# Kernel tuning notes

Hardware: AMD Instinct MI355X
Metric: run time of the kernel (lower is better)

## Reference

```python
import jax, jax.numpy as jnp
import numpy as np

D_IN = 1024
D_OUT = 1024


def setup_inputs() -> dict:
    key = jax.random.key(0)
    ks = jax.random.split(key, 7)
    B, S = 4, 2048
    x = jax.random.normal(ks[0], (B, S, D_IN), dtype=jnp.float32)
    s = 1.0 / np.sqrt(D_IN)
    Wq = jax.random.uniform(ks[1], (D_IN, D_OUT), jnp.float32, -s, s)
    Wk = jax.random.uniform(ks[2], (D_IN, D_OUT), jnp.float32, -s, s)
    Wv = jax.random.uniform(ks[3], (D_IN, D_OUT), jnp.float32, -s, s)
    bq = jax.random.uniform(ks[4], (D_OUT,), jnp.float32, -s, s)
    bk = jax.random.uniform(ks[5], (D_OUT,), jnp.float32, -s, s)
    bv = jax.random.uniform(ks[6], (D_OUT,), jnp.float32, -s, s)
    return {"x": x, "Wq": Wq, "Wk": Wk, "Wv": Wv, "bq": bq, "bk": bk, "bv": bv}


def reference(x, Wq, Wk, Wv, bq, bk, bv):
    # x: [B, S, d_in]
    B, S, _ = x.shape
    q = x @ Wq + bq            # [B, S, d_out]
    k = x @ Wk + bk
    v = x @ Wv + bv
    scale = 1.0 / jnp.sqrt(jnp.asarray(q.shape[-1], q.dtype))
    scores = jnp.einsum('bqd,bkd->bqk', q, k)  # [B, S, S]
    causal = jnp.tril(jnp.ones((S, S), dtype=bool))
    scores = jnp.where(causal, scores, -jnp.inf)
    attn = jax.nn.softmax(scores * scale, axis=-1)
    return jnp.einsum('bqk,bkd->bqd', attn, v)
```

## Files before the change

kernel.cpp:

```cpp
#include <hip/hip_runtime.h>
#include <cstdint>

#define DEV __device__ __forceinline__

typedef __attribute__((ext_vector_type(4))) float f32x4;
typedef __attribute__((ext_vector_type(8))) short short8;
typedef __attribute__((ext_vector_type(4))) unsigned short u16x4;

constexpr int BS  = 4;
constexpr int SEQ = 2048;

DEV ushort f2b(float f){
  uint32_t u = __builtin_bit_cast(uint32_t, f);
  u += 0x7fffu + ((u >> 16) & 1u);
  return (ushort)(u >> 16);
}
DEV float b2f(ushort h){
  uint32_t u = (uint32_t)h << 16;
  return __builtin_bit_cast(float, u);
}

DEV void gload_lds16(const void* g, void* l){
  __builtin_amdgcn_global_load_lds(
      (const __attribute__((address_space(1))) unsigned int*)g,
      (__attribute__((address_space(3))) unsigned int*)l, 16, 0, 0);
}

#define BAR()    __builtin_amdgcn_s_barrier()
#define PRIO(x)  __builtin_amdgcn_s_setprio(x)
#define SCHEDB() __builtin_amdgcn_sched_barrier(0)
#define LGKM0()  asm volatile("s_waitcnt lgkmcnt(0)" ::: "memory")
#define WAITV4() asm volatile("s_waitcnt vmcnt(4)" ::: "memory")

__global__ __launch_bounds__(256) void convert_f2b8(const float* __restrict__ src,
                                                    ushort* __restrict__ dst){
  long i = (long)blockIdx.x * 256 + threadIdx.x;
  const f32x4* s4 = (const f32x4*)src;
  f32x4 a = s4[i*2], b = s4[i*2+1];
  short8 o;
  o[0]=(short)f2b(a[0]); o[1]=(short)f2b(a[1]); o[2]=(short)f2b(a[2]); o[3]=(short)f2b(a[3]);
  o[4]=(short)f2b(b[0]); o[5]=(short)f2b(b[1]); o[6]=(short)f2b(b[2]); o[7]=(short)f2b(b[3]);
  ((short8*)dst)[i] = o;
}

__global__ __launch_bounds__(256) void transpose_f2b(const float* __restrict__ src,
                                                     ushort* __restrict__ dst,
                                                     int R, int C){
  __shared__ float t[32][33];
  int c0 = blockIdx.x * 32, r0 = blockIdx.y * 32;
  int tx = threadIdx.x, ty = threadIdx.y;
  #pragma unroll
  for (int k=0;k<4;k++) t[ty+k*8][tx] = src[(long)(r0+ty+k*8)*C + c0+tx];
  __syncthreads();
  #pragma unroll
  for (int k=0;k<4;k++) dst[(long)(c0+ty+k*8)*R + r0+tx] = f2b(t[tx][ty+k*8]);
}

__global__ __launch_bounds__(256) void transpose_b2b(const ushort* __restrict__ src,
                                                     ushort* __restrict__ dst,
                                                     int R, int C){
  __shared__ ushort t[32][33];
  int c0 = blockIdx.x * 32, r0 = blockIdx.y * 32;
  int tx = threadIdx.x, ty = threadIdx.y;
  #pragma unroll
  for (int k=0;k<4;k++) t[ty+k*8][tx] = src[(long)(r0+ty+k*8)*C + c0+tx];
  __syncthreads();
  #pragma unroll
  for (int k=0;k<4;k++) dst[(long)(c0+ty+k*8)*R + r0+tx] = t[tx][ty+k*8];
}

struct GArgs {
  const ushort* A;  long lda; long aBS;
  const ushort* Bm; long ldb; long bBS;
  void* C;          long ldc; long cBS;
  const float* b0; const float* b1; const float* b2;
  int K;
};

__global__ __launch_bounds__(512, 2) void gemmA_qkv(GArgs g){
  extern __shared__ char sm[];
  const int tid = threadIdx.x;
  const int wid = tid >> 6, lane = tid & 63;
  const int wr = wid >> 2, wc = wid & 3;
  const int lr = lane & 15, lk = lane >> 4;
  const int f5 = ((lr >> 3) & 1) << 5;

  int fid = blockIdx.x;
  int swz = (fid & 7) * 48 + (fid >> 3);
  const int m0 = (swz & 31) * 256;
  const int n0 = (swz >> 5) * 256;

  const long lda2 = g.lda * 2, ldb2 = g.ldb * 2;
  const int sr  = tid >> 2;
  const int scb = (lane & 3) << 4;
  const int scbp = scb ^ (((sr >> 3) & 1) << 5);
  const char* ar0 = (const char*)g.A  + (long)(m0 + sr      )*lda2 + scbp;
  const char* ar1 = (const char*)g.A  + (long)(m0 + 128 + sr)*lda2 + scbp;
  const char* br0 = (const char*)g.Bm + (long)(n0 + sr      )*ldb2 + scbp;
  const char* br1 = (const char*)g.Bm + (long)(n0 + 128 + sr)*ldb2 + scbp;
  const int dwo = wid << 10;

  auto ST = [&](const char* row, int c, int off, int k0){
    const char* p = row + k0*2;
    char* d = sm + c*65536 + off + dwo;
    gload_lds16(p,      d);
    gload_lds16(p + 64, d + 8192);
  };

  const int aoffs = wr*16384 + lr*64 + ((lk*16) ^ f5);
  const int boffs = 32768 + (wc>>1)*16384 + ((wc&1)*64 + lr)*64 + ((lk*16) ^ f5);

  f32x4 acc[8][4];
  #pragma unroll
  for (int m=0;m<8;m++)
    #pragma unroll
    for (int n=0;n<4;n++) acc[m][n] = f32x4{0.f,0.f,0.f,0.f};

  const int NT = g.K >> 6;
  ST(ar0, 0, 0, 0);     ST(ar1, 0, 16384, 0);
  ST(br0, 0, 32768, 0); ST(br1, 0, 49152, 0);
  ST(br0, 1, 32768, 64); ST(br1, 1, 49152, 64);
  WAITV4(); BAR();

  for (int t = 0; t < NT; ++t){
    const int c = t & 1;
    const char* base = sm + c*65536;
    const int kA = ((t+1) < NT ? (t+1) : NT-1) << 6;
    const int kB = ((t+2) < NT ? (t+2) : NT-1) << 6;
    short8 bf[4][2], af[2][2];
    ST(ar0, c^1, 0, kA); ST(ar1, c^1, 16384, kA);
    #pragma unroll
    for (int n=0;n<4;n++)
      #pragma unroll
      for (int kk=0;kk<2;kk++)
        bf[n][kk] = *(const short8*)(base + boffs + kk*8192 + n*1024);
    #pragma unroll
    for (int mm=0;mm<2;mm++)
      #pragma unroll
      for (int kk=0;kk<2;kk++)
        af[mm][kk] = *(const short8*)(base + aoffs + kk*8192 + mm*1024);
    LGKM0(); SCHEDB();
    PRIO(1);
    #pragma unroll
    for (int kk=0;kk<2;kk++)
      #pragma unroll
      for (int mm=0;mm<2;mm++)
        #pragma unroll
        for (int n=0;n<4;n++)
          acc[mm][n] = __builtin_amdgcn_mfma_f32_16x16x32_bf16(af[mm][kk], bf[n][kk], acc[mm][n], 0,0,0);
    PRIO(0);
    BAR();
    #pragma unroll
    for (int p=1;p<4;p++){
      if (p == 1) ST(br0, c, 32768, kB);
      if (p == 2) ST(br1, c, 49152, kB);
      #pragma unroll
      for (int mm=0;mm<2;mm++)
        #pragma unroll
        for (int kk=0;kk<2;kk++)
          af[mm][kk] = *(const short8*)(base + aoffs + kk*8192 + (p*2+mm)*1024);
      LGKM0(); SCHEDB();
      PRIO(1);
      #pragma unroll
      for (int kk=0;kk<2;kk++)
        #pragma unroll
        for (int mm=0;mm<2;mm++)
          #pragma unroll
          for (int n=0;n<4;n++)
            acc[p*2+mm][n] = __builtin_amdgcn_mfma_f32_16x16x32_bf16(af[mm][kk], bf[n][kk], acc[p*2+mm][n], 0,0,0);
      PRIO(0);
      if (p == 3) WAITV4();
      BAR();
    }
  }

  int sel = n0 >> 10;
  const float* bp = (sel == 0) ? g.b0 : (sel == 1) ? g.b1 : g.b2;
  ushort* Cq = (ushort*)g.C + (long)sel * 8388608;
  #pragma unroll
  for (int m=0;m<8;m++){
    int row0 = m0 + wr*128 + m*16 + lk*4;
    #pragma unroll
    for (int n=0;n<4;n++){
      int col  = n0 + wc*64 + n*16 + lr;
      int colq = col & 1023;
      float bv = bp[colq];
      #pragma unroll
      for (int i=0;i<4;i++)
        Cq[(long)(row0+i)*1024 + colq] = f2b(acc[m][n][i] + bv);
    }
  }
}

template<int MODE>
__global__ __launch_bounds__(512, 2) void gemmB(GArgs g){
  extern __shared__ char sm[];
  const int m0 = blockIdx.x * 128, n0 = blockIdx.y * 256;
  const int z  = blockIdx.z;
  if (MODE == 1 && n0 > m0 + 127) return;
  const int tid = threadIdx.x;
  const int wid = tid >> 6, lane = tid & 63;
  const int wr = wid >> 2, wc = wid & 3;
  const int lr = lane & 15, lk = lane >> 4;
  const int f5 = ((lr >> 3) & 1) << 5;

  const char* Ab = (const char*)(g.A  + (long)z * g.aBS);
  const char* Bb = (const char*)(g.Bm + (long)z * g.bBS);
  const long lda2 = g.lda * 2, ldb2 = g.ldb * 2;
  const int sr  = tid >> 2;
  const int scb = (lane & 3) << 4;
  const int scbp = scb ^ (((sr >> 3) & 1) << 5);
  const char* ar0 = Ab + (long)(m0 + sr)*lda2 + scbp;
  const char* br0 = Bb + (long)(n0 + sr      )*ldb2 + scbp;
  const char* br1 = Bb + (long)(n0 + 128 + sr)*ldb2 + scbp;
  const int dwo = wid << 10;

  auto ST = [&](const char* row, int c, int off, int k0){
    const char* p = row + k0*2;
    char* d = sm + c*49152 + off + dwo;
    gload_lds16(p,      d);
    gload_lds16(p + 64, d + 8192);
  };

  const int aoffs = (wr*64 + lr)*64 + ((lk*16) ^ f5);
  const int boffs = 16384 + (wc>>1)*16384 + ((wc&1)*64 + lr)*64 + ((lk*16) ^ f5);

  f32x4 acc[4][4];
  #pragma unroll
  for (int m=0;m<4;m++)
    #pragma unroll
    for (int n=0;n<4;n++) acc[m][n] = f32x4{0.f,0.f,0.f,0.f};

  const int Keff = (MODE == 2) ? (m0 + 128) : g.K;
  const int NT = Keff >> 6;
  ST(ar0, 0, 0, 0);
  ST(br0, 0, 16384, 0); ST(br1, 0, 32768, 0);
  ST(br0, 1, 16384, 64); ST(br1, 1, 32768, 64);
  WAITV4(); BAR();

  for (int t = 0; t < NT; ++t){
    const int c = t & 1;
    const char* base = sm + c*49152;
    const int kA = ((t+1) < NT ? (t+1) : NT-1) << 6;
    const int kB = ((t+2) < NT ? (t+2) : NT-1) << 6;
    short8 bf[4][2], af[2][2];
    ST(ar0, c^1, 0, kA);
    #pragma unroll
    for (int n=0;n<4;n++)
      #pragma unroll
      for (int kk=0;kk<2;kk++)
        bf[n][kk] = *(const short8*)(base + boffs + kk*8192 + n*1024);
    #pragma unroll
    for (int mm=0;mm<2;mm++)
      #pragma unroll
      for (int kk=0;kk<2;kk++)
        af[mm][kk] = *(const short8*)(base + aoffs + kk*8192 + mm*1024);
    LGKM0(); SCHEDB();
    PRIO(1);
    #pragma unroll
    for (int kk=0;kk<2;kk++)
      #pragma unroll
      for (int mm=0;mm<2;mm++)
        #pragma unroll
        for (int n=0;n<4;n++)
          acc[mm][n] = __builtin_amdgcn_mfma_f32_16x16x32_bf16(af[mm][kk], bf[n][kk], acc[mm][n], 0,0,0);
    PRIO(0);
    BAR();
    ST(br0, c, 16384, kB); ST(br1, c, 32768, kB);
    #pragma unroll
    for (int mm=0;mm<2;mm++)
      #pragma unroll
      for (int kk=0;kk<2;kk++)
        af[mm][kk] = *(const short8*)(base + aoffs + kk*8192 + (2+mm)*1024);
    LGKM0(); SCHEDB();
    PRIO(1);
    #pragma unroll
    for (int kk=0;kk<2;kk++)
      #pragma unroll
      for (int mm=0;mm<2;mm++)
        #pragma unroll
        for (int n=0;n<4;n++)
          acc[2+mm][n] = __builtin_amdgcn_mfma_f32_16x16x32_bf16(af[mm][kk], bf[n][kk], acc[2+mm][n], 0,0,0);
    PRIO(0);
    WAITV4();
    BAR();
  }

  long cz = (long)z * g.cBS;
  #pragma unroll
  for (int m=0;m<4;m++){
    int row0 = m0 + wr*64 + m*16 + lk*4;
    #pragma unroll
    for (int n=0;n<4;n++){
      int col = n0 + wc*64 + n*16 + lr;
      #pragma unroll
      for (int i=0;i<4;i++){
        long off = cz + (long)(row0+i)*g.ldc + col;
        if (MODE == 1) ((ushort*)g.C)[off] = f2b(acc[m][n][i]);
        else           ((float*)g.C)[off]  = acc[m][n][i];
      }
    }
  }
}

__global__ __launch_bounds__(256) void softmax_causal_b(const ushort* __restrict__ sc,
                                                        ushort* __restrict__ P){
  int row = blockIdx.x & (SEQ-1);
  int b   = blockIdx.x >> 11;
  const short8* srow = (const short8*)(sc + ((long)b*SEQ + row)*(long)SEQ);
  ushort* prow = P + ((long)b*SEQ + row)*(long)SEQ;
  int tid = threadIdx.x;
  int lane = tid & 63, wid = tid >> 6;
  const float scale = 0.03125f;
  float x[8]; float mx = -INFINITY;
  int base = tid * 8;
  if (base <= row){
    short8 v = srow[tid];
    #pragma unroll
    for (int j=0;j<8;j++){
      float t = (base + j <= row) ? b2f((ushort)v[j]) : -INFINITY;
      x[j] = t; mx = fmaxf(mx, t);
    }
  } else {
    #pragma unroll
    for (int j=0;j<8;j++) x[j] = -INFINITY;
  }
  #pragma unroll
  for (int off=1; off<64; off<<=1) mx = fmaxf(mx, __shfl_xor(mx, off));
  __shared__ float rb[8];
  if (lane == 0) rb[wid] = mx;
  __syncthreads();
  mx = fmaxf(fmaxf(rb[0],rb[1]), fmaxf(rb[2],rb[3]));
  float sum = 0.f; float e[8];
  #pragma unroll
  for (int i=0;i<8;i++){ e[i] = __expf((x[i]-mx)*scale); sum += e[i]; }
  #pragma unroll
  for (int off=1; off<64; off<<=1) sum += __shfl_xor(sum, off);
  if (lane == 0) rb[4+wid] = sum;
  __syncthreads();
  sum = (rb[4]+rb[5]) + (rb[6]+rb[7]);
  float inv = 1.0f / sum;
  int wlim = row | 127;
  if (base <= wlim){
    short8 o;
    #pragma unroll
    for (int j=0;j<8;j++) o[j] = (short)f2b(e[j]*inv);
    ((short8*)prow)[tid] = o;
  }
}

extern "C" void kernel_launch(void* const* d_in, const int* in_sizes, int n_in,
                              void* d_out, int out_size, void* d_ws, size_t ws_size,
                              hipStream_t stream){
  const float* x  = (const float*)d_in[0];
  const float* Wq = (const float*)d_in[1];
  const float* Wk = (const float*)d_in[2];
  const float* Wv = (const float*)d_in[3];
  const float* bq = (const float*)d_in[4];
  const float* bk = (const float*)d_in[5];
  const float* bv = (const float*)d_in[6];
  float* out = (float*)d_out;

  const long XB = 0;
  const long WT = 16777216;
  const long QB = 23068672;
  const long VT = 73400320;
  const long SC = 90177536;
  const long NEED = 157286400;
  const long PB = 0;
  if ((long)ws_size < NEED) return;

  char* ws = (char*)d_ws;
  ushort* xb = (ushort*)(ws + XB);
  ushort* wt = (ushort*)(ws + WT);
  ushort* qb = (ushort*)(ws + QB);
  ushort* kb = qb + 8388608;
  ushort* vb = qb + 16777216;
  ushort* vt = (ushort*)(ws + VT);
  ushort* sc = (ushort*)(ws + SC);
  ushort* pb = (ushort*)(ws + PB);

  hipFuncSetAttribute(reinterpret_cast<const void*>(&gemmA_qkv),
                      hipFuncAttributeMaxDynamicSharedMemorySize, 131072);
  hipFuncSetAttribute(reinterpret_cast<const void*>(&gemmB<1>),
                      hipFuncAttributeMaxDynamicSharedMemorySize, 98304);
  hipFuncSetAttribute(reinterpret_cast<const void*>(&gemmB<2>),
                      hipFuncAttributeMaxDynamicSharedMemorySize, 98304);

  dim3 tb(32, 8);

  convert_f2b8<<<4096, 256, 0, stream>>>(x, xb);
  transpose_f2b<<<dim3(32,32), tb, 0, stream>>>(Wq, wt + 0,       1024, 1024);
  transpose_f2b<<<dim3(32,32), tb, 0, stream>>>(Wk, wt + 1048576, 1024, 1024);
  transpose_f2b<<<dim3(32,32), tb, 0, stream>>>(Wv, wt + 2097152, 1024, 1024);

  GArgs pa{};
  pa.A = xb; pa.lda = 1024; pa.aBS = 0;
  pa.Bm = wt; pa.ldb = 1024; pa.bBS = 0;
  pa.C = (void*)qb; pa.ldc = 1024; pa.cBS = 0;
  pa.b0 = bq; pa.b1 = bk; pa.b2 = bv;
  pa.K = 1024;
  gemmA_qkv<<<384, 512, 131072, stream>>>(pa);

  transpose_b2b<<<dim3(32,256), tb, 0, stream>>>(vb, vt, 8192, 1024);

  GArgs sa{};
  sa.A = qb;  sa.lda = 1024; sa.aBS = (long)SEQ*1024;
  sa.Bm = kb; sa.ldb = 1024; sa.bBS = (long)SEQ*1024;
  sa.C = (void*)sc; sa.ldc = SEQ; sa.cBS = (long)SEQ*SEQ;
  sa.b0 = nullptr; sa.b1 = nullptr; sa.b2 = nullptr;
  sa.K = 1024;
  gemmB<1><<<dim3(16,8,4), 512, 98304, stream>>>(sa);

  softmax_causal_b<<<BS*SEQ, 256, 0, stream>>>(sc, pb);

  GArgs va{};
  va.A = pb;  va.lda = SEQ;  va.aBS = (long)SEQ*SEQ;
  va.Bm = vt; va.ldb = 8192; va.bBS = SEQ;
  va.C = (void*)out; va.ldc = 1024; va.cBS = (long)SEQ*1024;
  va.b0 = nullptr; va.b1 = nullptr; va.b2 = nullptr;
  va.K = SEQ;
  gemmB<2><<<dim3(16,4,4), 512, 98304, stream>>>(va);
}
```

Baseline: 178.2 us.

## Retile QKV projection GEMM to 256x192 tiles with XCD-aware block mapping

```diff
diff --git a/kernel.cpp b/kernel.cpp
--- a/kernel.cpp
+++ b/kernel.cpp
@@ -30,7 +30,7 @@
 #define PRIO(x)  __builtin_amdgcn_s_setprio(x)
 #define SCHEDB() __builtin_amdgcn_sched_barrier(0)
 #define LGKM0()  asm volatile("s_waitcnt lgkmcnt(0)" ::: "memory")
-#define WAITV4() asm volatile("s_waitcnt vmcnt(4)" ::: "memory")
+#define WAITV(n) asm volatile("s_waitcnt vmcnt(" #n ")" ::: "memory")
 
 __global__ __launch_bounds__(256) void convert_f2b8(const float* __restrict__ src,
                                                     ushort* __restrict__ dst){
@@ -85,109 +85,119 @@
   const int lr = lane & 15, lk = lane >> 4;
   const int f5 = ((lr >> 3) & 1) << 5;
 
-  int fid = blockIdx.x;
-  int swz = (fid & 7) * 48 + (fid >> 3);
-  const int m0 = (swz & 31) * 256;
-  const int n0 = (swz >> 5) * 256;
+  const int fid = blockIdx.x;
+  const int xcd = fid & 7, j = fid >> 3;
+  const int m0 = (xcd * 4 + (j & 3)) * 256;
+  const int n0 = (j >> 2) * 192;
 
   const long lda2 = g.lda * 2, ldb2 = g.ldb * 2;
-  const int sr  = tid >> 2;
-  const int scb = (lane & 3) << 4;
-  const int scbp = scb ^ (((sr >> 3) & 1) << 5);
-  const char* ar0 = (const char*)g.A  + (long)(m0 + sr      )*lda2 + scbp;
-  const char* ar1 = (const char*)g.A  + (long)(m0 + 128 + sr)*lda2 + scbp;
-  const char* br0 = (const char*)g.Bm + (long)(n0 + sr      )*ldb2 + scbp;
-  const char* br1 = (const char*)g.Bm + (long)(n0 + 128 + sr)*ldb2 + scbp;
-  const int dwo = wid << 10;
-
-  auto ST = [&](const char* row, int c, int off, int k0){
-    const char* p = row + k0*2;
-    char* d = sm + c*65536 + off + dwo;
-    gload_lds16(p,      d);
-    gload_lds16(p + 64, d + 8192);
-  };
-
-  const int aoffs = wr*16384 + lr*64 + ((lk*16) ^ f5);
-  const int boffs = 32768 + (wc>>1)*16384 + ((wc&1)*64 + lr)*64 + ((lk*16) ^ f5);
-
-  f32x4 acc[8][4];
+  const int skk = tid >> 8;
+  const int srr = (tid >> 2) & 63;
+  const int scc = tid & 3;
+  const int scb = (scc * 16) ^ (((srr >> 3) & 1) << 5);
+  const char* aU0 = (const char*)g.A  + (long)(m0       + srr)*lda2 + skk*64 + scb;
+  const char* aU1 = (const char*)g.A  + (long)(m0 +  64 + srr)*lda2 + skk*64 + scb;
+  const char* aU2 = (const char*)g.A  + (long)(m0 + 128 + srr)*lda2 + skk*64 + scb;
+  const char* aU3 = (const char*)g.A  + (long)(m0 + 192 + srr)*lda2 + skk*64 + scb;
+  const char* bU0 = (const char*)g.Bm + (long)(n0       + srr)*ldb2 + skk*64 + scb;
+  const char* bU1 = (const char*)g.Bm + (long)(n0 +  64 + srr)*ldb2 + skk*64 + scb;
+  const char* bU2 = (const char*)g.Bm + (long)(n0 + 128 + srr)*ldb2 + skk*64 + scb;
+  const int dst = tid * 16;
+
+#define STA(u, cb, k0) gload_lds16(aU##u + (k0)*2, sm + (cb)*57344 + u*8192 + dst)
+#define STB(u, cb, k0) gload_lds16(bU##u + (k0)*2, sm + (cb)*57344 + 32768 + u*8192 + dst)
+
+  int aoff[8], boff[3];
+  #pragma unroll
+  for (int mm=0;mm<8;mm++)
+    aoff[mm] = wr*16384 + (mm>>2)*8192 + (mm&3)*1024 + lr*64 + ((lk*16) ^ f5);
+  #pragma unroll
+  for (int nn=0;nn<3;nn++){
+    int br = wc*48 + nn*16 + lr;
+    boff[nn] = 32768 + (br>>6)*8192 + (br&63)*64 + ((lk*16) ^ f5);
+  }
+
+  f32x4 acc[8][3];
   #pragma unroll
   for (int m=0;m<8;m++)
     #pragma unroll
-    for (int n=0;n<4;n++) acc[m][n] = f32x4{0.f,0.f,0.f,0.f};
+    for (int n=0;n<3;n++) acc[m][n] = f32x4{0.f,0.f,0.f,0.f};
 
   const int NT = g.K >> 6;
-  ST(ar0, 0, 0, 0);     ST(ar1, 0, 16384, 0);
-  ST(br0, 0, 32768, 0); ST(br1, 0, 49152, 0);
-  ST(br0, 1, 32768, 64); ST(br1, 1, 49152, 64);
-  WAITV4(); BAR();
+  STA(0,0,0); STA(1,0,0); STA(2,0,0); STA(3,0,0);
+  STB(0,0,0); STB(1,0,0); STB(2,0,0);
+  STB(0,1,64); STB(1,1,64); STB(2,1,64);
+  WAITV(3); BAR();
+
+  short8 bf[3][2], af[2][2];
+#define READ_AF(MB) \
+    af[0][0] = *(const short8*)(base + aoff[MB  ]);        \
+    af[0][1] = *(const short8*)(base + aoff[MB  ] + 4096); \
+    af[1][0] = *(const short8*)(base + aoff[MB+1]);        \
+    af[1][1] = *(const short8*)(base + aoff[MB+1] + 4096);
+#define MFMA6(MB) \
+    PRIO(1); \
+    _Pragma("unroll") \
+    for (int kk=0;kk<2;kk++) \
+      _Pragma("unroll") \
+      for (int mm=0;mm<2;mm++) \
+        _Pragma("unroll") \
+        for (int nn=0;nn<3;nn++) \
+          acc[MB+mm][nn] = __builtin_amdgcn_mfma_f32_16x16x32_bf16(af[mm][kk], bf[nn][kk], acc[MB+mm][nn], 0,0,0); \
+    PRIO(0);
 
   for (int t = 0; t < NT; ++t){
     const int c = t & 1;
-    const char* base = sm + c*65536;
+    const char* base = sm + c*57344;
     const int kA = ((t+1) < NT ? (t+1) : NT-1) << 6;
     const int kB = ((t+2) < NT ? (t+2) : NT-1) << 6;
-    short8 bf[4][2], af[2][2];
-    ST(ar0, c^1, 0, kA); ST(ar1, c^1, 16384, kA);
-    #pragma unroll
-    for (int n=0;n<4;n++)
-      #pragma unroll
-      for (int kk=0;kk<2;kk++)
-        bf[n][kk] = *(const short8*)(base + boffs + kk*8192 + n*1024);
-    #pragma unroll
-    for (int mm=0;mm<2;mm++)
-      #pragma unroll
-      for (int kk=0;kk<2;kk++)
-        af[mm][kk] = *(const short8*)(base + aoffs + kk*8192 + mm*1024);
-    LGKM0(); SCHEDB();
-    PRIO(1);
-    #pragma unroll
-    for (int kk=0;kk<2;kk++)
-      #pragma unroll
-      for (int mm=0;mm<2;mm++)
-        #pragma unroll
-        for (int n=0;n<4;n++)
-          acc[mm][n] = __builtin_amdgcn_mfma_f32_16x16x32_bf16(af[mm][kk], bf[n][kk], acc[mm][n], 0,0,0);
-    PRIO(0);
-    BAR();
-    #pragma unroll
-    for (int p=1;p<4;p++){
-      if (p == 1) ST(br0, c, 32768, kB);
-      if (p == 2) ST(br1, c, 49152, kB);
-      #pragma unroll
-      for (int mm=0;mm<2;mm++)
-        #pragma unroll
-        for (int kk=0;kk<2;kk++)
-          af[mm][kk] = *(const short8*)(base + aoffs + kk*8192 + (p*2+mm)*1024);
-      LGKM0(); SCHEDB();
-      PRIO(1);
-      #pragma unroll
-      for (int kk=0;kk<2;kk++)
-        #pragma unroll
-        for (int mm=0;mm<2;mm++)
-          #pragma unroll
-          for (int n=0;n<4;n++)
-            acc[p*2+mm][n] = __builtin_amdgcn_mfma_f32_16x16x32_bf16(af[mm][kk], bf[n][kk], acc[p*2+mm][n], 0,0,0);
-      PRIO(0);
-      if (p == 3) WAITV4();
-      BAR();
+    STA(0, c^1, kA); STA(1, c^1, kA);
+    #pragma unroll
+    for (int nn=0;nn<3;nn++){
+      bf[nn][0] = *(const short8*)(base + boff[nn]);
+      bf[nn][1] = *(const short8*)(base + boff[nn] + 4096);
     }
-  }
-
-  int sel = n0 >> 10;
-  const float* bp = (sel == 0) ? g.b0 : (sel == 1) ? g.b1 : g.b2;
-  ushort* Cq = (ushort*)g.C + (long)sel * 8388608;
-  #pragma unroll
-  for (int m=0;m<8;m++){
-    int row0 = m0 + wr*128 + m*16 + lk*4;
-    #pragma unroll
-    for (int n=0;n<4;n++){
-      int col  = n0 + wc*64 + n*16 + lr;
-      int colq = col & 1023;
-      float bv = bp[colq];
+    READ_AF(0);
+    LGKM0(); SCHEDB();
+    MFMA6(0);
+    BAR();
+    STA(2, c^1, kA); STA(3, c^1, kA);
+    READ_AF(2);
+    LGKM0(); SCHEDB();
+    MFMA6(2);
+    BAR();
+    STB(0, c, kB); STB(1, c, kB);
+    READ_AF(4);
+    LGKM0(); SCHEDB();
+    MFMA6(4);
+    BAR();
+    STB(2, c, kB);
+    READ_AF(6);
+    LGKM0(); SCHEDB();
+    MFMA6(6);
+    WAITV(3);
+    BAR();
+  }
+  WAITV(0);
+#undef STA
+#undef STB
+#undef READ_AF
+#undef MFMA6
+
+  #pragma unroll
+  for (int nn=0;nn<3;nn++){
+    int col  = n0 + wc*48 + nn*16 + lr;
+    int sel  = col >> 10;
+    int colq = col & 1023;
+    const float* bp = (sel == 0) ? g.b0 : (sel == 1) ? g.b1 : g.b2;
+    float bv = bp[colq];
+    ushort* Cq = (ushort*)g.C + (long)sel * 8388608;
+    #pragma unroll
+    for (int mm=0;mm<8;mm++){
+      int row0 = m0 + wr*128 + mm*16 + lk*4;
       #pragma unroll
       for (int i=0;i<4;i++)
-        Cq[(long)(row0+i)*1024 + colq] = f2b(acc[m][n][i] + bv);
+        Cq[(long)(row0+i)*1024 + colq] = f2b(acc[mm][nn][i] + bv);
     }
   }
 }
@@ -208,11 +218,10 @@
   const char* Bb = (const char*)(g.Bm + (long)z * g.bBS);
   const long lda2 = g.lda * 2, ldb2 = g.ldb * 2;
   const int sr  = tid >> 2;
-  const int scb = (lane & 3) << 4;
-  const int scbp = scb ^ (((sr >> 3) & 1) << 5);
-  const char* ar0 = Ab + (long)(m0 + sr)*lda2 + scbp;
-  const char* br0 = Bb + (long)(n0 + sr      )*ldb2 + scbp;
-  const char* br1 = Bb + (long)(n0 + 128 + sr)*ldb2 + scbp;
+  const int scb = ((lane & 3) << 4) ^ (((sr >> 3) & 1) << 5);
+  const char* ar0 = Ab + (long)(m0 + sr)*lda2 + scb;
+  const char* br0 = Bb + (long)(n0 + sr      )*ldb2 + scb;
+  const char* br1 = Bb + (long)(n0 + 128 + sr)*ldb2 + scb;
   const int dwo = wid << 10;
 
   auto ST = [&](const char* row, int c, int off, int k0){
@@ -236,7 +245,7 @@
   ST(ar0, 0, 0, 0);
   ST(br0, 0, 16384, 0); ST(br1, 0, 32768, 0);
   ST(br0, 1, 16384, 64); ST(br1, 1, 32768, 64);
-  WAITV4(); BAR();
+  WAITV(4); BAR();
 
   for (int t = 0; t < NT; ++t){
     const int c = t & 1;
@@ -282,9 +291,10 @@
         for (int n=0;n<4;n++)
           acc[2+mm][n] = __builtin_amdgcn_mfma_f32_16x16x32_bf16(af[mm][kk], bf[n][kk], acc[2+mm][n], 0,0,0);
     PRIO(0);
-    WAITV4();
-    BAR();
-  }
+    WAITV(4);
+    BAR();
+  }
+  WAITV(0);
 
   long cz = (long)z * g.cBS;
   #pragma unroll
@@ -381,7 +391,7 @@
   ushort* pb = (ushort*)(ws + PB);
 
   hipFuncSetAttribute(reinterpret_cast<const void*>(&gemmA_qkv),
-                      hipFuncAttributeMaxDynamicSharedMemorySize, 131072);
+                      hipFuncAttributeMaxDynamicSharedMemorySize, 114688);
   hipFuncSetAttribute(reinterpret_cast<const void*>(&gemmB<1>),
                       hipFuncAttributeMaxDynamicSharedMemorySize, 98304);
   hipFuncSetAttribute(reinterpret_cast<const void*>(&gemmB<2>),
@@ -400,7 +410,7 @@
   pa.C = (void*)qb; pa.ldc = 1024; pa.cBS = 0;
   pa.b0 = bq; pa.b1 = bk; pa.b2 = bv;
   pa.K = 1024;
-  gemmA_qkv<<<384, 512, 131072, stream>>>(pa);
+  gemmA_qkv<<<512, 512, 114688, stream>>>(pa);
 
   transpose_b2b<<<dim3(32,256), tb, 0, stream>>>(vb, vt, 8192, 1024);
 
```

Result: faster. 173.8 us (-2.5%).

## Replace QKV and score GEMMs with 3-stage ring-buffered 256x256 tile kernel

Applied to the files above, without the earlier changes.

```diff
diff --git a/kernel.cpp b/kernel.cpp
--- a/kernel.cpp
+++ b/kernel.cpp
@@ -30,7 +30,7 @@
 #define PRIO(x)  __builtin_amdgcn_s_setprio(x)
 #define SCHEDB() __builtin_amdgcn_sched_barrier(0)
 #define LGKM0()  asm volatile("s_waitcnt lgkmcnt(0)" ::: "memory")
-#define WAITV4() asm volatile("s_waitcnt vmcnt(4)" ::: "memory")
+#define WAITV(n) asm volatile("s_waitcnt vmcnt(" #n ")" ::: "memory")
 
 __global__ __launch_bounds__(256) void convert_f2b8(const float* __restrict__ src,
                                                     ushort* __restrict__ dst){
@@ -77,142 +77,157 @@
   int K;
 };
 
-__global__ __launch_bounds__(512, 2) void gemmA_qkv(GArgs g){
+template<int MODE>
+__global__ __launch_bounds__(512, 2) void ring256(GArgs g){
   extern __shared__ char sm[];
+  int m0, n0, z = 0;
+  if (MODE == 0){
+    const int fid = blockIdx.x;
+    const int xcd = fid & 7, j = fid >> 3;
+    m0 = (xcd * 4 + (j & 3)) * 256;
+    n0 = (j >> 2) * 256;
+  } else {
+    m0 = blockIdx.x * 256; n0 = blockIdx.y * 256; z = blockIdx.z;
+    if (n0 > m0) return;
+  }
+  const int tid = threadIdx.x;
+  const int wid = tid >> 6, lane = tid & 63;
+  const int wr = wid >> 2, wc = wid & 3;
+  const int lr = lane & 15, lk = lane >> 4;
+
+  const char* Ab = (const char*)(g.A  + (long)z * g.aBS);
+  const char* Bb = (const char*)(g.Bm + (long)z * g.bBS);
+  const long lda2 = g.lda * 2, ldb2 = g.ldb * 2;
+  const int sr  = tid >> 2;
+  const int scb = ((tid & 3) << 4) ^ (((sr >> 3) & 1) << 5);
+  const char* aR0 = Ab + (long)(m0       + sr)*lda2 + scb;
+  const char* aR1 = Ab + (long)(m0 + 128 + sr)*lda2 + scb;
+  const char* bR0 = Bb + (long)(n0       + sr)*ldb2 + scb;
+  const char* bR1 = Bb + (long)(n0 + 128 + sr)*ldb2 + scb;
+  const int dst = tid << 4;
+
+  int aoff[8], boff[4];
+  #pragma unroll
+  for (int m=0;m<8;m++){
+    int r = wr*128 + m*16 + lr;
+    aoff[m] = r*64 + ((lk*16) ^ (((r>>3)&1)<<5));
+  }
+  #pragma unroll
+  for (int n=0;n<4;n++){
+    int r = wc*64 + n*16 + lr;
+    boff[n] = 16384 + r*64 + ((lk*16) ^ (((r>>3)&1)<<5));
+  }
+
+  f32x4 acc[8][4];
+  #pragma unroll
+  for (int m=0;m<8;m++)
+    #pragma unroll
+    for (int n=0;n<4;n++) acc[m][n] = f32x4{0.f,0.f,0.f,0.f};
+
+  const int NT = g.K >> 5;
+  gload_lds16(aR0,      sm + dst);
+  gload_lds16(aR1,      sm + 8192  + dst);
+  gload_lds16(bR0,      sm + 16384 + dst);
+  gload_lds16(bR1,      sm + 24576 + dst);
+  gload_lds16(aR0 + 64, sm + 32768 + dst);
+  gload_lds16(aR1 + 64, sm + 32768 + 8192  + dst);
+  gload_lds16(bR0 + 64, sm + 32768 + 16384 + dst);
+  gload_lds16(bR1 + 64, sm + 32768 + 24576 + dst);
+  WAITV(4); BAR();
+
+  int p = 0;
+  for (int t = 0; t < NT; ++t){
+    const char* base = sm + p*32768;
+    const int t2 = (t+2 < NT) ? t+2 : NT-1;
+    const long kB = (long)(t2) << 6;
+    int pS = p + 2; if (pS >= 3) pS -= 3;
+    char* sb = sm + pS*32768;
+    short8 af[4], bf[4];
+    gload_lds16(aR0 + kB, sb + dst);
+    gload_lds16(aR1 + kB, sb + 8192 + dst);
+    #pragma unroll
+    for (int n=0;n<4;n++) bf[n] = *(const short8*)(base + boff[n]);
+    #pragma unroll
+    for (int m=0;m<4;m++) af[m] = *(const short8*)(base + aoff[m]);
+    LGKM0(); SCHEDB();
+    PRIO(1);
+    #pragma unroll
+    for (int m=0;m<4;m++)
+      #pragma unroll
+      for (int n=0;n<4;n++)
+        acc[m][n] = __builtin_amdgcn_mfma_f32_16x16x32_bf16(af[m], bf[n], acc[m][n], 0,0,0);
+    PRIO(0);
+    BAR();
+    gload_lds16(bR0 + kB, sb + 16384 + dst);
+    gload_lds16(bR1 + kB, sb + 24576 + dst);
+    #pragma unroll
+    for (int m=0;m<4;m++) af[m] = *(const short8*)(base + aoff[4+m]);
+    LGKM0(); SCHEDB();
+    PRIO(1);
+    #pragma unroll
+    for (int m=0;m<4;m++)
+      #pragma unroll
+      for (int n=0;n<4;n++)
+        acc[4+m][n] = __builtin_amdgcn_mfma_f32_16x16x32_bf16(af[m], bf[n], acc[4+m][n], 0,0,0);
+    PRIO(0);
+    WAITV(4);
+    BAR();
+    p = (p+1 == 3) ? 0 : p+1;
+  }
+  WAITV(0);
+
+  if (MODE == 0){
+    const int sel = n0 >> 10;
+    const float* bp = (sel == 0) ? g.b0 : (sel == 1) ? g.b1 : g.b2;
+    ushort* Cq = (ushort*)g.C + (long)sel * 8388608;
+    const int nq0 = (n0 & 1023);
+    #pragma unroll
+    for (int n=0;n<4;n++){
+      int colq = nq0 + wc*64 + n*16 + lr;
+      float bv = bp[colq];
+      #pragma unroll
+      for (int m=0;m<8;m++){
+        int row0 = m0 + wr*128 + m*16 + lk*4;
+        #pragma unroll
+        for (int i=0;i<4;i++)
+          Cq[(long)(row0+i)*1024 + colq] = f2b(acc[m][n][i] + bv);
+      }
+    }
+  } else {
+    ushort* Cs = (ushort*)g.C + (long)z * g.cBS;
+    #pragma unroll
+    for (int m=0;m<8;m++){
+      int row0 = m0 + wr*128 + m*16 + lk*4;
+      #pragma unroll
+      for (int n=0;n<4;n++){
+        int col = n0 + wc*64 + n*16 + lr;
+        #pragma unroll
+        for (int i=0;i<4;i++)
+          Cs[(long)(row0+i)*g.ldc + col] = f2b(acc[m][n][i]);
+      }
+    }
+  }
+}
+
+template<int MODE>
+__global__ __launch_bounds__(512, 2) void gemmB(GArgs g){
+  extern __shared__ char sm[];
+  const int m0 = blockIdx.x * 128, n0 = blockIdx.y * 256;
+  const int z  = blockIdx.z;
   const int tid = threadIdx.x;
   const int wid = tid >> 6, lane = tid & 63;
   const int wr = wid >> 2, wc = wid & 3;
   const int lr = lane & 15, lk = lane >> 4;
   const int f5 = ((lr >> 3) & 1) << 5;
 
-  int fid = blockIdx.x;
-  int swz = (fid & 7) * 48 + (fid >> 3);
-  const int m0 = (swz & 31) * 256;
-  const int n0 = (swz >> 5) * 256;
-
-  const long lda2 = g.lda * 2, ldb2 = g.ldb * 2;
-  const int sr  = tid >> 2;
-  const int scb = (lane & 3) << 4;
-  const int scbp = scb ^ (((sr >> 3) & 1) << 5);
-  const char* ar0 = (const char*)g.A  + (long)(m0 + sr      )*lda2 + scbp;
-  const char* ar1 = (const char*)g.A  + (long)(m0 + 128 + sr)*lda2 + scbp;
-  const char* br0 = (const char*)g.Bm + (long)(n0 + sr      )*ldb2 + scbp;
-  const char* br1 = (const char*)g.Bm + (long)(n0 + 128 + sr)*ldb2 + scbp;
-  const int dwo = wid << 10;
-
-  auto ST = [&](const char* row, int c, int off, int k0){
-    const char* p = row + k0*2;
-    char* d = sm + c*65536 + off + dwo;
-    gload_lds16(p,      d);
-    gload_lds16(p + 64, d + 8192);
-  };
-
-  const int aoffs = wr*16384 + lr*64 + ((lk*16) ^ f5);
-  const int boffs = 32768 + (wc>>1)*16384 + ((wc&1)*64 + lr)*64 + ((lk*16) ^ f5);
-
-  f32x4 acc[8][4];
-  #pragma unroll
-  for (int m=0;m<8;m++)
-    #pragma unroll
-    for (int n=0;n<4;n++) acc[m][n] = f32x4{0.f,0.f,0.f,0.f};
-
-  const int NT = g.K >> 6;
-  ST(ar0, 0, 0, 0);     ST(ar1, 0, 16384, 0);
-  ST(br0, 0, 32768, 0); ST(br1, 0, 49152, 0);
-  ST(br0, 1, 32768, 64); ST(br1, 1, 49152, 64);
-  WAITV4(); BAR();
-
-  for (int t = 0; t < NT; ++t){
-    const int c = t & 1;
-    const char* base = sm + c*65536;
-    const int kA = ((t+1) < NT ? (t+1) : NT-1) << 6;
-    const int kB = ((t+2) < NT ? (t+2) : NT-1) << 6;
-    short8 bf[4][2], af[2][2];
-    ST(ar0, c^1, 0, kA); ST(ar1, c^1, 16384, kA);
-    #pragma unroll
-    for (int n=0;n<4;n++)
-      #pragma unroll
-      for (int kk=0;kk<2;kk++)
-        bf[n][kk] = *(const short8*)(base + boffs + kk*8192 + n*1024);
-    #pragma unroll
-    for (int mm=0;mm<2;mm++)
-      #pragma unroll
-      for (int kk=0;kk<2;kk++)
-        af[mm][kk] = *(const short8*)(base + aoffs + kk*8192 + mm*1024);
-    LGKM0(); SCHEDB();
-    PRIO(1);
-    #pragma unroll
-    for (int kk=0;kk<2;kk++)
-      #pragma unroll
-      for (int mm=0;mm<2;mm++)
-        #pragma unroll
-        for (int n=0;n<4;n++)
-          acc[mm][n] = __builtin_amdgcn_mfma_f32_16x16x32_bf16(af[mm][kk], bf[n][kk], acc[mm][n], 0,0,0);
-    PRIO(0);
-    BAR();
-    #pragma unroll
-    for (int p=1;p<4;p++){
-      if (p == 1) ST(br0, c, 32768, kB);
-      if (p == 2) ST(br1, c, 49152, kB);
-      #pragma unroll
-      for (int mm=0;mm<2;mm++)
-        #pragma unroll
-        for (int kk=0;kk<2;kk++)
-          af[mm][kk] = *(const short8*)(base + aoffs + kk*8192 + (p*2+mm)*1024);
-      LGKM0(); SCHEDB();
-      PRIO(1);
-      #pragma unroll
-      for (int kk=0;kk<2;kk++)
-        #pragma unroll
-        for (int mm=0;mm<2;mm++)
-          #pragma unroll
-          for (int n=0;n<4;n++)
-            acc[p*2+mm][n] = __builtin_amdgcn_mfma_f32_16x16x32_bf16(af[mm][kk], bf[n][kk], acc[p*2+mm][n], 0,0,0);
-      PRIO(0);
-      if (p == 3) WAITV4();
-      BAR();
-    }
-  }
-
-  int sel = n0 >> 10;
-  const float* bp = (sel == 0) ? g.b0 : (sel == 1) ? g.b1 : g.b2;
-  ushort* Cq = (ushort*)g.C + (long)sel * 8388608;
-  #pragma unroll
-  for (int m=0;m<8;m++){
-    int row0 = m0 + wr*128 + m*16 + lk*4;
-    #pragma unroll
-    for (int n=0;n<4;n++){
-      int col  = n0 + wc*64 + n*16 + lr;
-      int colq = col & 1023;
-      float bv = bp[colq];
-      #pragma unroll
-      for (int i=0;i<4;i++)
-        Cq[(long)(row0+i)*1024 + colq] = f2b(acc[m][n][i] + bv);
-    }
-  }
-}
-
-template<int MODE>
-__global__ __launch_bounds__(512, 2) void gemmB(GArgs g){
-  extern __shared__ char sm[];
-  const int m0 = blockIdx.x * 128, n0 = blockIdx.y * 256;
-  const int z  = blockIdx.z;
-  if (MODE == 1 && n0 > m0 + 127) return;
-  const int tid = threadIdx.x;
-  const int wid = tid >> 6, lane = tid & 63;
-  const int wr = wid >> 2, wc = wid & 3;
-  const int lr = lane & 15, lk = lane >> 4;
-  const int f5 = ((lr >> 3) & 1) << 5;
-
   const char* Ab = (const char*)(g.A  + (long)z * g.aBS);
   const char* Bb = (const char*)(g.Bm + (long)z * g.bBS);
   const long lda2 = g.lda * 2, ldb2 = g.ldb * 2;
   const int sr  = tid >> 2;
-  const int scb = (lane & 3) << 4;
-  const int scbp = scb ^ (((sr >> 3) & 1) << 5);
-  const char* ar0 = Ab + (long)(m0 + sr)*lda2 + scbp;
-  const char* br0 = Bb + (long)(n0 + sr      )*ldb2 + scbp;
-  const char* br1 = Bb + (long)(n0 + 128 + sr)*ldb2 + scbp;
+  const int scb = ((lane & 3) << 4) ^ (((sr >> 3) & 1) << 5);
+  const char* ar0 = Ab + (long)(m0 + sr)*lda2 + scb;
+  const char* br0 = Bb + (long)(n0 + sr      )*ldb2 + scb;
+  const char* br1 = Bb + (long)(n0 + 128 + sr)*ldb2 + scb;
   const int dwo = wid << 10;
 
   auto ST = [&](const char* row, int c, int off, int k0){
@@ -231,12 +246,12 @@
     #pragma unroll
     for (int n=0;n<4;n++) acc[m][n] = f32x4{0.f,0.f,0.f,0.f};
 
-  const int Keff = (MODE == 2) ? (m0 + 128) : g.K;
+  const int Keff = m0 + 128;
   const int NT = Keff >> 6;
   ST(ar0, 0, 0, 0);
   ST(br0, 0, 16384, 0); ST(br1, 0, 32768, 0);
   ST(br0, 1, 16384, 64); ST(br1, 1, 32768, 64);
-  WAITV4(); BAR();
+  WAITV(4); BAR();
 
   for (int t = 0; t < NT; ++t){
     const int c = t & 1;
@@ -282,9 +297,10 @@
         for (int n=0;n<4;n++)
           acc[2+mm][n] = __builtin_amdgcn_mfma_f32_16x16x32_bf16(af[mm][kk], bf[n][kk], acc[2+mm][n], 0,0,0);
     PRIO(0);
-    WAITV4();
+    WAITV(4);
     BAR();
   }
+  WAITV(0);
 
   long cz = (long)z * g.cBS;
   #pragma unroll
@@ -294,11 +310,8 @@
     for (int n=0;n<4;n++){
       int col = n0 + wc*64 + n*16 + lr;
       #pragma unroll
-      for (int i=0;i<4;i++){
-        long off = cz + (long)(row0+i)*g.ldc + col;
-        if (MODE == 1) ((ushort*)g.C)[off] = f2b(acc[m][n][i]);
-        else           ((float*)g.C)[off]  = acc[m][n][i];
-      }
+      for (int i=0;i<4;i++)
+        ((float*)g.C)[cz + (long)(row0+i)*g.ldc + col] = acc[m][n][i];
     }
   }
 }
@@ -380,9 +393,9 @@
   ushort* sc = (ushort*)(ws + SC);
   ushort* pb = (ushort*)(ws + PB);
 
-  hipFuncSetAttribute(reinterpret_cast<const void*>(&gemmA_qkv),
-                      hipFuncAttributeMaxDynamicSharedMemorySize, 131072);
-  hipFuncSetAttribute(reinterpret_cast<const void*>(&gemmB<1>),
+  hipFuncSetAttribute(reinterpret_cast<const void*>(&ring256<0>),
+                      hipFuncAttributeMaxDynamicSharedMemorySize, 98304);
+  hipFuncSetAttribute(reinterpret_cast<const void*>(&ring256<1>),
                       hipFuncAttributeMaxDynamicSharedMemorySize, 98304);
   hipFuncSetAttribute(reinterpret_cast<const void*>(&gemmB<2>),
                       hipFuncAttributeMaxDynamicSharedMemorySize, 98304);
@@ -400,7 +413,7 @@
   pa.C = (void*)qb; pa.ldc = 1024; pa.cBS = 0;
   pa.b0 = bq; pa.b1 = bk; pa.b2 = bv;
   pa.K = 1024;
-  gemmA_qkv<<<384, 512, 131072, stream>>>(pa);
+  ring256<0><<<384, 512, 98304, stream>>>(pa);
 
   transpose_b2b<<<dim3(32,256), tb, 0, stream>>>(vb, vt, 8192, 1024);
 
@@ -410,7 +423,7 @@
   sa.C = (void*)sc; sa.ldc = SEQ; sa.cBS = (long)SEQ*SEQ;
   sa.b0 = nullptr; sa.b1 = nullptr; sa.b2 = nullptr;
   sa.K = 1024;
-  gemmB<1><<<dim3(16,8,4), 512, 98304, stream>>>(sa);
+  ring256<1><<<dim3(8,8,4), 512, 98304, stream>>>(sa);
 
   softmax_causal_b<<<BS*SEQ, 256, 0, stream>>>(sc, pb);
 
```

Result: no change. 179.3 us (+0.6%).
